# Kernel tuning notes

Measured on AMD Instinct MI355X. Metric: run time of the kernel, lower is better.

Reference implementation:

```python
import jax, jax.numpy as jnp
import numpy as np

B, NQ, NK = 4, 2048, 2048
D_MODEL, D_K, D_V, H = 1024, 1024, 1024, 16


def setup_inputs() -> dict:
    key = jax.random.key(0)
    ks = jax.random.split(key, 8)
    return {
        "queries": jax.random.normal(ks[0], (B, NQ, D_MODEL), dtype=jnp.float32),
        "keys": jax.random.normal(ks[1], (B, NK, D_MODEL), dtype=jnp.float32),
        "values": jax.random.normal(ks[2], (B, NK, D_MODEL), dtype=jnp.float32),
        # nn.Linear weights init.normal_(std=0.001); stored here in (in, out) layout
        "Wq": jax.random.normal(ks[3], (D_MODEL, D_K), dtype=jnp.float32) * 0.001,
        "Wk": jax.random.normal(ks[4], (D_MODEL, D_K), dtype=jnp.float32) * 0.001,
        "Wv": jax.random.normal(ks[5], (D_MODEL, D_V), dtype=jnp.float32) * 0.001,
        "Wo": jax.random.normal(ks[6], (D_V, D_MODEL), dtype=jnp.float32) * 0.001,
        "bo": jnp.zeros((D_MODEL,), dtype=jnp.float32),
    }


def reference(queries, keys, values, Wq, Wk, Wv, Wo, bo):
    b_s, nq, _ = queries.shape
    nk = keys.shape[1]
    hd_k = D_K // H  # per-head key dim
    hd_v = D_V // H  # per-head value dim
    # projections -> [b, h, n, hd]
    q = (queries @ Wq).reshape(b_s, nq, H, hd_k).transpose(0, 2, 1, 3)
    k = (keys @ Wk).reshape(b_s, nk, H, hd_k).transpose(0, 2, 1, 3)
    v = (values @ Wv).reshape(b_s, nk, H, hd_v).transpose(0, 2, 1, 3)
    # NOTE: original scales by sqrt(d_k) (full d_k), not per-head dim
    att = jnp.einsum("bhqd,bhkd->bhqk", q, k) / np.float32(np.sqrt(D_K))
    att = jax.nn.softmax(att, axis=-1)
    # dropout = identity (eval mode)
    out = jnp.einsum("bhqk,bhkd->bhqd", att, v)
    out = out.transpose(0, 2, 1, 3).reshape(b_s, nq, D_V)
    return out @ Wo + bo
```

## Files before the change

kernel.cpp:

```cpp
#include <hip/hip_runtime.h>


#define DM    1024
#define NSEQ  2048
#define HEADS 16
#define HD    64

typedef float floatx4 __attribute__((ext_vector_type(4)));
typedef short s16x4   __attribute__((ext_vector_type(4)));
typedef short s16x8   __attribute__((ext_vector_type(8)));
typedef unsigned int u32x4 __attribute__((ext_vector_type(4)));

static __device__ __forceinline__ floatx4 mfma_bf16(s16x8 a, s16x8 b, floatx4 c) {
  return __builtin_amdgcn_mfma_f32_16x16x32_bf16(a, b, c, 0, 0, 0);
}

static __device__ __forceinline__ void gload_lds16(const void* g, void* l) {
  __builtin_amdgcn_global_load_lds(
      (const __attribute__((address_space(1))) unsigned*)g,
      (__attribute__((address_space(3))) unsigned*)l, 16, 0, 0);
}

static __device__ __forceinline__ short f2bf(float f) {
  unsigned u = __builtin_bit_cast(unsigned, f);
  u += 0x7FFFu + ((u >> 16) & 1u);
  return (short)(u >> 16);
}

static __device__ __forceinline__ unsigned pack2_bf16(float a, float b) {
  unsigned ua = __builtin_bit_cast(unsigned, a) + 0x8000u;
  unsigned ub = __builtin_bit_cast(unsigned, b) + 0x8000u;
#if __has_builtin(__builtin_amdgcn_perm)
  return __builtin_amdgcn_perm(ub, ua, 0x07060302u);
#else
  return (ub & 0xffff0000u) | (ua >> 16);
#endif
}

__global__ __launch_bounds__(256) void transpose_cast_w(
    const float* __restrict__ W0, const float* __restrict__ W1,
    const float* __restrict__ W2, const float* __restrict__ W3,
    short* __restrict__ T0, short* __restrict__ T1,
    short* __restrict__ T2, short* __restrict__ T3) {
  __shared__ float tile[32][33];
  const float* W = blockIdx.z == 0 ? W0 : blockIdx.z == 1 ? W1 : blockIdx.z == 2 ? W2 : W3;
  short*       T = blockIdx.z == 0 ? T0 : blockIdx.z == 1 ? T1 : blockIdx.z == 2 ? T2 : T3;
  const int bx = blockIdx.x * 32;
  const int by = blockIdx.y * 32;
  const int tx = threadIdx.x, ty = threadIdx.y;
  for (int i = 0; i < 4; i++)
    tile[ty + i * 8][tx] = W[(long)(by + ty + i * 8) * DM + bx + tx];
  __syncthreads();
  for (int i = 0; i < 4; i++)
    T[(long)(bx + ty + i * 8) * DM + by + tx] = f2bf(tile[tx][ty + i * 8]);
}

__global__ __launch_bounds__(256) void proj_kernel(
    const float* __restrict__ Aq, const float* __restrict__ Ak, const float* __restrict__ Av,
    const short* __restrict__ BtQ, const short* __restrict__ BtK, const short* __restrict__ BtV,
    short* __restrict__ Qh, short* __restrict__ Kh, short* __restrict__ Vt) {
  __shared__ short As[128 * 40];
  __shared__ short Bs[128 * 40];
  const int z = blockIdx.z;
  const float* A  = z == 0 ? Aq  : z == 1 ? Ak  : Av;
  const short* Bt = z == 0 ? BtQ : z == 1 ? BtK : BtV;
  const int t = threadIdx.x;
  const int w = t >> 6, l = t & 63, quad = l >> 4, lm = l & 15;
  const int wm = w >> 1, wn = w & 1;
  const int row0 = blockIdx.x * 128, col0 = blockIdx.y * 128;

  floatx4 acc[4][4];
  for (int mi = 0; mi < 4; mi++)
    for (int ni = 0; ni < 4; ni++) acc[mi][ni] = (floatx4){0.f, 0.f, 0.f, 0.f};

  for (int k0 = 0; k0 < DM; k0 += 32) {
    for (int j = 0; j < 4; j++) {
      int idx = j * 256 + t;
      int row = idx >> 3, c4 = idx & 7;
      floatx4 v = *(const floatx4*)(A + (long)(row0 + row) * DM + k0 + c4 * 4);
      s16x4 hv = {f2bf(v[0]), f2bf(v[1]), f2bf(v[2]), f2bf(v[3])};
      *(s16x4*)(As + row * 40 + c4 * 4) = hv;
    }
    for (int j = 0; j < 2; j++) {
      int idx = j * 256 + t;
      int row = idx >> 2, ch = idx & 3;
      *(s16x8*)(Bs + row * 40 + ch * 8) =
          *(const s16x8*)(Bt + (long)(col0 + row) * DM + k0 + ch * 8);
    }
    __syncthreads();
    s16x8 af[4], bfr[4];
    for (int mi = 0; mi < 4; mi++)
      af[mi] = *(const s16x8*)(As + (wm * 64 + mi * 16 + lm) * 40 + quad * 8);
    for (int ni = 0; ni < 4; ni++)
      bfr[ni] = *(const s16x8*)(Bs + (wn * 64 + ni * 16 + lm) * 40 + quad * 8);
    for (int mi = 0; mi < 4; mi++)
      for (int ni = 0; ni < 4; ni++)
        acc[mi][ni] = mfma_bf16(af[mi], bfr[ni], acc[mi][ni]);
    __syncthreads();
  }

  const int rowbase = row0 + wm * 64;
  const int colbase = col0 + wn * 64;
  const int b = rowbase >> 11;
  const int h = colbase >> 6;
  const int rloc = rowbase & 2047;
  if (z < 2) {
    short* Out = z == 0 ? Qh : Kh;
    const float osc = z == 0 ? 0.0450842200277801f : 1.0f;
    long base = ((long)(b * HEADS + h)) * NSEQ * HD;
    for (int mi = 0; mi < 4; mi++)
      for (int r = 0; r < 4; r++) {
        int q = rloc + mi * 16 + quad * 4 + r;
        long rowoff = base + (long)q * HD + lm;
        for (int ni = 0; ni < 4; ni++)
          Out[rowoff + ni * 16] = f2bf(acc[mi][ni][r] * osc);
      }
  } else {
    long base = ((long)(b * HEADS + h)) * HD * NSEQ;
    for (int mi = 0; mi < 4; mi++)
      for (int r = 0; r < 4; r++) {
        int kcol = rloc + (mi >> 1) * 32 + quad * 8 + (mi & 1) * 4 + r;
        for (int ni = 0; ni < 4; ni++)
          Vt[base + (long)(ni * 16 + lm) * NSEQ + kcol] = f2bf(acc[mi][ni][r]);
      }
  }
}

__global__ __launch_bounds__(256, 2) void attn_kernel(
    const short* __restrict__ Qh, const short* __restrict__ Kh,
    const short* __restrict__ Vt, short* __restrict__ Obf) {
  __shared__ short lds[2 * 8192];
  const int t = threadIdx.x;
  const int w = t >> 6, l = t & 63, quad = l >> 4, lm = l & 15;
  const int bh = blockIdx.x;
  const int qtile = blockIdx.y * 128 + w * 32;
  const short* Qp = Qh + (long)bh * NSEQ * HD;
  const short* Kp = Kh + (long)bh * NSEQ * HD;
  const short* Vp = Vt + (long)bh * HD * NSEQ;

  s16x8 aq[2][2];
#pragma unroll
  for (int qi = 0; qi < 2; qi++)
#pragma unroll
    for (int c = 0; c < 2; c++)
      aq[qi][c] = *(const s16x8*)(Qp + (long)(qtile + qi * 16 + lm) * HD + c * 32 + quad * 8);

  floatx4 acc[2][4];
  float lsum[2] = {0.f, 0.f};
#pragma unroll
  for (int qi = 0; qi < 2; qi++)
#pragma unroll
    for (int n = 0; n < 4; n++) acc[qi][n] = (floatx4){0.f, 0.f, 0.f, 0.f};

  auto stage = [&](int kt, int buf) __attribute__((always_inline)) {
    short* base = lds + buf * 8192;
#pragma unroll
    for (int i = 0; i < 4; i++) {
      int g = w * 4 + i;
      const short* src;
      if (w < 2) {
        int s = (g >> 2) & 1, j = (g >> 1) & 1, c = g & 1;
        src = Kp + (long)(kt + s * 32 + j * 16 + lm) * HD + c * 32 + quad * 8;
      } else {
        int gg = g & 7;
        int s = gg >> 2, n = gg & 3;
        src = Vp + (long)(n * 16 + lm) * NSEQ + kt + s * 32 + quad * 8;
      }
      gload_lds16(src, base + g * 512);
    }
  };

  auto process = [&](const short* Lb, int s) __attribute__((always_inline)) {
    s16x8 bk[2][2];
#pragma unroll
    for (int j = 0; j < 2; j++)
#pragma unroll
      for (int c = 0; c < 2; c++)
        bk[j][c] = *(const s16x8*)(Lb + ((s * 4 + j * 2 + c) * 64 + l) * 8);
    s16x8 vraw[4];
#pragma unroll
    for (int n = 0; n < 4; n++)
      vraw[n] = *(const s16x8*)(Lb + ((8 + s * 4 + n) * 64 + l) * 8);
#pragma unroll
    for (int qi = 0; qi < 2; qi++) {
      floatx4 sT[2];
      sT[0] = (floatx4){0.f, 0.f, 0.f, 0.f};
      sT[1] = (floatx4){0.f, 0.f, 0.f, 0.f};
      __builtin_amdgcn_s_setprio(1);
#pragma unroll
      for (int c = 0; c < 2; c++) {
        sT[0] = mfma_bf16(bk[0][c], aq[qi][c], sT[0]);
        sT[1] = mfma_bf16(bk[1][c], aq[qi][c], sT[1]);
      }
      __builtin_amdgcn_s_setprio(0);
      float p0 = __builtin_amdgcn_exp2f(sT[0][0]);
      float p1 = __builtin_amdgcn_exp2f(sT[0][1]);
      float p2 = __builtin_amdgcn_exp2f(sT[0][2]);
      float p3 = __builtin_amdgcn_exp2f(sT[0][3]);
      float p4 = __builtin_amdgcn_exp2f(sT[1][0]);
      float p5 = __builtin_amdgcn_exp2f(sT[1][1]);
      float p6 = __builtin_amdgcn_exp2f(sT[1][2]);
      float p7 = __builtin_amdgcn_exp2f(sT[1][3]);
      lsum[qi] += ((p0 + p1) + (p2 + p3)) + ((p4 + p5) + (p6 + p7));
      u32x4 pw = {pack2_bf16(p0, p1), pack2_bf16(p2, p3),
                  pack2_bf16(p4, p5), pack2_bf16(p6, p7)};
      s16x8 pcat = __builtin_bit_cast(s16x8, pw);
      __builtin_amdgcn_s_setprio(1);
#pragma unroll
      for (int n = 0; n < 4; n++)
        acc[qi][n] = mfma_bf16(vraw[n], pcat, acc[qi][n]);
      __builtin_amdgcn_s_setprio(0);
    }
  };

  stage(0, 0);
  __syncthreads();
  int cur = 0;
  for (int kt = 0; kt < NSEQ; kt += 64) {
    if (kt + 64 < NSEQ) stage(kt + 64, cur ^ 1);
    const short* Lb = lds + cur * 8192;
    process(Lb, 0);
    process(Lb, 1);
    __syncthreads();
    cur ^= 1;
  }

  const int b = bh >> 4, h = bh & 15;
  short* Ow = lds + w * 1152;
  const int erow = l >> 2, ecg = l & 3;
#pragma unroll
  for (int qi = 0; qi < 2; qi++) {
    float ls = lsum[qi];
    ls += __shfl_xor(ls, 16);
    ls += __shfl_xor(ls, 32);
    float rl = 1.0f / ls;
#pragma unroll
    for (int n = 0; n < 4; n++)
#pragma unroll
      for (int r = 0; r < 4; r++)
        Ow[lm * 72 + n * 16 + quad * 4 + r] = f2bf(acc[qi][n][r] * rl);
    s16x8 o0 = *(const s16x8*)(Ow + erow * 72 + ecg * 16);
    s16x8 o1 = *(const s16x8*)(Ow + erow * 72 + ecg * 16 + 8);
    long gaddr = ((long)(b * NSEQ + qtile + qi * 16 + erow)) * DM + h * HD + ecg * 16;
    *(s16x8*)(Obf + gaddr) = o0;
    *(s16x8*)(Obf + gaddr + 8) = o1;
  }
}

__global__ __launch_bounds__(256) void out_kernel(
    const short* __restrict__ Ab, const short* __restrict__ Bt,
    const float* __restrict__ bias, float* __restrict__ Out) {
  __shared__ short As[128 * 40];
  __shared__ short Bs[128 * 40];
  const int t = threadIdx.x;
  const int w = t >> 6, l = t & 63, quad = l >> 4, lm = l & 15;
  const int wm = w >> 1, wn = w & 1;
  const int row0 = blockIdx.x * 128, col0 = blockIdx.y * 128;

  floatx4 acc[4][4];
  for (int mi = 0; mi < 4; mi++)
    for (int ni = 0; ni < 4; ni++) acc[mi][ni] = (floatx4){0.f, 0.f, 0.f, 0.f};

  for (int k0 = 0; k0 < DM; k0 += 32) {
    for (int j = 0; j < 2; j++) {
      int idx = j * 256 + t;
      int row = idx >> 2, ch = idx & 3;
      *(s16x8*)(As + row * 40 + ch * 8) =
          *(const s16x8*)(Ab + (long)(row0 + row) * DM + k0 + ch * 8);
    }
    for (int j = 0; j < 2; j++) {
      int idx = j * 256 + t;
      int row = idx >> 2, ch = idx & 3;
      *(s16x8*)(Bs + row * 40 + ch * 8) =
          *(const s16x8*)(Bt + (long)(col0 + row) * DM + k0 + ch * 8);
    }
    __syncthreads();
    s16x8 af[4], bfr[4];
    for (int mi = 0; mi < 4; mi++)
      af[mi] = *(const s16x8*)(As + (wm * 64 + mi * 16 + lm) * 40 + quad * 8);
    for (int ni = 0; ni < 4; ni++)
      bfr[ni] = *(const s16x8*)(Bs + (wn * 64 + ni * 16 + lm) * 40 + quad * 8);
    for (int mi = 0; mi < 4; mi++)
      for (int ni = 0; ni < 4; ni++)
        acc[mi][ni] = mfma_bf16(af[mi], bfr[ni], acc[mi][ni]);
    __syncthreads();
  }

  const int rowbase = row0 + wm * 64;
  const int colbase = col0 + wn * 64;
  for (int mi = 0; mi < 4; mi++)
    for (int r = 0; r < 4; r++) {
      int gr = rowbase + mi * 16 + quad * 4 + r;
      for (int ni = 0; ni < 4; ni++) {
        int gc = colbase + ni * 16 + lm;
        Out[(long)gr * DM + gc] = acc[mi][ni][r] + bias[gc];
      }
    }
}

extern "C" void kernel_launch(void* const* d_in, const int* in_sizes, int n_in,
                              void* d_out, int out_size, void* d_ws, size_t ws_size,
                              hipStream_t stream) {
  (void)in_sizes; (void)n_in; (void)out_size; (void)ws_size;
  const float* queries = (const float*)d_in[0];
  const float* keys    = (const float*)d_in[1];
  const float* values  = (const float*)d_in[2];
  const float* Wq = (const float*)d_in[3];
  const float* Wk = (const float*)d_in[4];
  const float* Wv = (const float*)d_in[5];
  const float* Wo = (const float*)d_in[6];
  const float* bo = (const float*)d_in[7];
  float* out = (float*)d_out;

  char* ws = (char*)d_ws;
  const size_t MB = 1024 * 1024;
  short* WqT = (short*)(ws + 0 * MB);
  short* WkT = (short*)(ws + 2 * MB);
  short* WvT = (short*)(ws + 4 * MB);
  short* WoT = (short*)(ws + 6 * MB);
  short* Qh  = (short*)(ws + 8 * MB);
  short* Kh  = (short*)(ws + 24 * MB);
  short* Vt  = (short*)(ws + 40 * MB);
  short* Obf = (short*)(ws + 56 * MB);

  transpose_cast_w<<<dim3(32, 32, 4), dim3(32, 8), 0, stream>>>(
      Wq, Wk, Wv, Wo, WqT, WkT, WvT, WoT);
  proj_kernel<<<dim3(64, 8, 3), 256, 0, stream>>>(
      queries, keys, values, WqT, WkT, WvT, Qh, Kh, Vt);
  attn_kernel<<<dim3(64, 16), 256, 0, stream>>>(Qh, Kh, Vt, Obf);
  out_kernel<<<dim3(64, 8), 256, 0, stream>>>(Obf, WoT, bo, out);
}
```

Baseline: 368.7 us.

## Double-buffer projection and output GEMMs with direct global-to-LDS loads

Measured after the change: 389.6 us. +5.7%, slower.

```diff
diff --git a/kernel.cpp b/kernel.cpp
--- a/kernel.cpp
+++ b/kernel.cpp
@@ -25,6 +25,12 @@
   unsigned u = __builtin_bit_cast(unsigned, f);
   u += 0x7FFFu + ((u >> 16) & 1u);
   return (short)(u >> 16);
+}
+
+static __device__ __forceinline__ unsigned cvtpk_bf16(float lo, float hi) {
+  unsigned r;
+  asm("v_cvt_pk_bf16_f32 %0, %1, %2" : "=v"(r) : "v"(lo), "v"(hi));
+  return r;
 }
 
 static __device__ __forceinline__ unsigned pack2_bf16(float a, float b) {
@@ -55,12 +61,11 @@
     T[(long)(bx + ty + i * 8) * DM + by + tx] = f2bf(tile[tx][ty + i * 8]);
 }
 
-__global__ __launch_bounds__(256) void proj_kernel(
+__global__ __launch_bounds__(256, 2) void proj_kernel(
     const float* __restrict__ Aq, const float* __restrict__ Ak, const float* __restrict__ Av,
     const short* __restrict__ BtQ, const short* __restrict__ BtK, const short* __restrict__ BtV,
     short* __restrict__ Qh, short* __restrict__ Kh, short* __restrict__ Vt) {
-  __shared__ short As[128 * 40];
-  __shared__ short Bs[128 * 40];
+  __shared__ short lds[2 * 8192];
   const int z = blockIdx.z;
   const float* A  = z == 0 ? Aq  : z == 1 ? Ak  : Av;
   const short* Bt = z == 0 ? BtQ : z == 1 ? BtK : BtV;
@@ -73,30 +78,70 @@
   for (int mi = 0; mi < 4; mi++)
     for (int ni = 0; ni < 4; ni++) acc[mi][ni] = (floatx4){0.f, 0.f, 0.f, 0.f};
 
-  for (int k0 = 0; k0 < DM; k0 += 32) {
-    for (int j = 0; j < 4; j++) {
-      int idx = j * 256 + t;
-      int row = idx >> 3, c4 = idx & 7;
-      floatx4 v = *(const floatx4*)(A + (long)(row0 + row) * DM + k0 + c4 * 4);
-      s16x4 hv = {f2bf(v[0]), f2bf(v[1]), f2bf(v[2]), f2bf(v[3])};
-      *(s16x4*)(As + row * 40 + c4 * 4) = hv;
-    }
-    for (int j = 0; j < 2; j++) {
-      int idx = j * 256 + t;
-      int row = idx >> 2, ch = idx & 3;
-      *(s16x8*)(Bs + row * 40 + ch * 8) =
-          *(const s16x8*)(Bt + (long)(col0 + row) * DM + k0 + ch * 8);
-    }
-    __syncthreads();
+  floatx4 ar[4];
+  auto loadA = [&](int k0) __attribute__((always_inline)) {
+    {
+      int c = t, g = c >> 6, q = (c >> 4) & 3, rm = c & 15;
+      const float* p = A + (long)(row0 + g * 16 + rm) * DM + k0 + q * 8;
+      ar[0] = *(const floatx4*)p;
+      ar[1] = *(const floatx4*)(p + 4);
+    }
+    {
+      int c = t + 256, g = c >> 6, q = (c >> 4) & 3, rm = c & 15;
+      const float* p = A + (long)(row0 + g * 16 + rm) * DM + k0 + q * 8;
+      ar[2] = *(const floatx4*)p;
+      ar[3] = *(const floatx4*)(p + 4);
+    }
+  };
+  auto writeA = [&](int buf) __attribute__((always_inline)) {
+    short* base = lds + buf * 8192;
+    u32x4 w0 = {cvtpk_bf16(ar[0][0], ar[0][1]), cvtpk_bf16(ar[0][2], ar[0][3]),
+                cvtpk_bf16(ar[1][0], ar[1][1]), cvtpk_bf16(ar[1][2], ar[1][3])};
+    u32x4 w1 = {cvtpk_bf16(ar[2][0], ar[2][1]), cvtpk_bf16(ar[2][2], ar[2][3]),
+                cvtpk_bf16(ar[3][0], ar[3][1]), cvtpk_bf16(ar[3][2], ar[3][3])};
+    *(s16x8*)(base + t * 8)         = __builtin_bit_cast(s16x8, w0);
+    *(s16x8*)(base + (t + 256) * 8) = __builtin_bit_cast(s16x8, w1);
+  };
+  auto stageB = [&](int k0, int buf) __attribute__((always_inline)) {
+    short* base = lds + buf * 8192 + 4096;
+#pragma unroll
+    for (int i = 0; i < 2; i++) {
+      int g = w * 2 + i;
+      const short* src = Bt + (long)(col0 + g * 16 + lm) * DM + k0 + quad * 8;
+      gload_lds16(src, base + g * 512);
+    }
+  };
+  auto process = [&](int buf) __attribute__((always_inline)) {
+    const short* base = lds + buf * 8192;
     s16x8 af[4], bfr[4];
-    for (int mi = 0; mi < 4; mi++)
-      af[mi] = *(const s16x8*)(As + (wm * 64 + mi * 16 + lm) * 40 + quad * 8);
+#pragma unroll
+    for (int mi = 0; mi < 4; mi++)
+      af[mi] = *(const s16x8*)(base + (wm * 4 + mi) * 512 + l * 8);
+#pragma unroll
     for (int ni = 0; ni < 4; ni++)
-      bfr[ni] = *(const s16x8*)(Bs + (wn * 64 + ni * 16 + lm) * 40 + quad * 8);
-    for (int mi = 0; mi < 4; mi++)
+      bfr[ni] = *(const s16x8*)(base + 4096 + (wn * 4 + ni) * 512 + l * 8);
+    __builtin_amdgcn_s_setprio(1);
+#pragma unroll
+    for (int mi = 0; mi < 4; mi++)
+#pragma unroll
       for (int ni = 0; ni < 4; ni++)
         acc[mi][ni] = mfma_bf16(af[mi], bfr[ni], acc[mi][ni]);
+    __builtin_amdgcn_s_setprio(0);
+  };
+
+  loadA(0);
+  stageB(0, 0);
+  writeA(0);
+  __syncthreads();
+  int cur = 0;
+  for (int k0 = 0; k0 < DM; k0 += 32) {
+    const int kn = (k0 + 32 < DM) ? k0 + 32 : 0;
+    loadA(kn);
+    stageB(kn, cur ^ 1);
+    process(cur);
+    writeA(cur ^ 1);
     __syncthreads();
+    cur ^= 1;
   }
 
   const int rowbase = row0 + wm * 64;
@@ -247,11 +292,10 @@
   }
 }
 
-__global__ __launch_bounds__(256) void out_kernel(
+__global__ __launch_bounds__(256, 2) void out_kernel(
     const short* __restrict__ Ab, const short* __restrict__ Bt,
     const float* __restrict__ bias, float* __restrict__ Out) {
-  __shared__ short As[128 * 40];
-  __shared__ short Bs[128 * 40];
+  __shared__ short lds[2 * 8192];
   const int t = threadIdx.x;
   const int w = t >> 6, l = t & 63, quad = l >> 4, lm = l & 15;
   const int wm = w >> 1, wn = w & 1;
@@ -261,29 +305,44 @@
   for (int mi = 0; mi < 4; mi++)
     for (int ni = 0; ni < 4; ni++) acc[mi][ni] = (floatx4){0.f, 0.f, 0.f, 0.f};
 
-  for (int k0 = 0; k0 < DM; k0 += 32) {
-    for (int j = 0; j < 2; j++) {
-      int idx = j * 256 + t;
-      int row = idx >> 2, ch = idx & 3;
-      *(s16x8*)(As + row * 40 + ch * 8) =
-          *(const s16x8*)(Ab + (long)(row0 + row) * DM + k0 + ch * 8);
-    }
-    for (int j = 0; j < 2; j++) {
-      int idx = j * 256 + t;
-      int row = idx >> 2, ch = idx & 3;
-      *(s16x8*)(Bs + row * 40 + ch * 8) =
-          *(const s16x8*)(Bt + (long)(col0 + row) * DM + k0 + ch * 8);
-    }
-    __syncthreads();
+  auto stage = [&](int k0, int buf) __attribute__((always_inline)) {
+    short* base = lds + buf * 8192;
+#pragma unroll
+    for (int i = 0; i < 4; i++) {
+      int g = w * 4 + i;
+      const short* src = (g < 8)
+          ? Ab + (long)(row0 + g * 16 + lm) * DM + k0 + quad * 8
+          : Bt + (long)(col0 + (g - 8) * 16 + lm) * DM + k0 + quad * 8;
+      gload_lds16(src, base + g * 512);
+    }
+  };
+  auto process = [&](int buf) __attribute__((always_inline)) {
+    const short* base = lds + buf * 8192;
     s16x8 af[4], bfr[4];
-    for (int mi = 0; mi < 4; mi++)
-      af[mi] = *(const s16x8*)(As + (wm * 64 + mi * 16 + lm) * 40 + quad * 8);
+#pragma unroll
+    for (int mi = 0; mi < 4; mi++)
+      af[mi] = *(const s16x8*)(base + (wm * 4 + mi) * 512 + l * 8);
+#pragma unroll
     for (int ni = 0; ni < 4; ni++)
-      bfr[ni] = *(const s16x8*)(Bs + (wn * 64 + ni * 16 + lm) * 40 + quad * 8);
-    for (int mi = 0; mi < 4; mi++)
+      bfr[ni] = *(const s16x8*)(base + (8 + wn * 4 + ni) * 512 + l * 8);
+    __builtin_amdgcn_s_setprio(1);
+#pragma unroll
+    for (int mi = 0; mi < 4; mi++)
+#pragma unroll
       for (int ni = 0; ni < 4; ni++)
         acc[mi][ni] = mfma_bf16(af[mi], bfr[ni], acc[mi][ni]);
+    __builtin_amdgcn_s_setprio(0);
+  };
+
+  stage(0, 0);
+  __syncthreads();
+  int cur = 0;
+  for (int k0 = 0; k0 < DM; k0 += 32) {
+    const int kn = (k0 + 32 < DM) ? k0 + 32 : 0;
+    stage(kn, cur ^ 1);
+    process(cur);
     __syncthreads();
+    cur ^= 1;
   }
 
   const int rowbase = row0 + wm * 64;
```
